# Kernel tuning notes

Hardware: AMD Instinct MI355X
Metric: run time of the kernel (lower is better)

Reference implementation:

```python
import jax, jax.numpy as jnp
import numpy as np

N = 20000
IN_CH, HID, OUT_CH = 512, 64, 16
H1, H2 = 8, 1
NEG_SLOPE = 0.2


def setup_inputs() -> dict:
    key = jax.random.key(0)
    ks = jax.random.split(key, 10)
    E = 320000
    x = jax.random.normal(ks[0], (N, IN_CH), dtype=jnp.float32)
    edge_index = jax.random.randint(ks[1], (2, E), 0, N, dtype=jnp.int64)
    s = 0.05
    return {
        "x": x,
        "edge_index": edge_index,
        "W1": jax.random.normal(ks[2], (H1 * HID, IN_CH), dtype=jnp.float32) * s,
        "att_src1": jax.random.normal(ks[3], (1, H1, HID), dtype=jnp.float32) * s,
        "att_dst1": jax.random.normal(ks[4], (1, H1, HID), dtype=jnp.float32) * s,
        "b1": jnp.zeros((H1 * HID,), dtype=jnp.float32),
        "W2": jax.random.normal(ks[5], (H2 * OUT_CH, H1 * HID), dtype=jnp.float32) * s,
        "att_src2": jax.random.normal(ks[6], (1, H2, OUT_CH), dtype=jnp.float32) * s,
        "att_dst2": jax.random.normal(ks[7], (1, H2, OUT_CH), dtype=jnp.float32) * s,
        "b2": jnp.zeros((OUT_CH,), dtype=jnp.float32),
    }


def _gat_conv(x, src, dst, W, att_src, att_dst, bias, heads, out_ch, concat):
    # Linear transform: [N, H, C]
    h = (x @ W.T).reshape(x.shape[0], heads, out_ch)
    n = x.shape[0]
    # Per-node attention logits (a_src . h), (a_dst . h): [N, H]
    a_s = (h * att_src).sum(-1)
    a_d = (h * att_dst).sum(-1)
    # Edge-wise LeakyReLU attention: [E, H]
    e = a_s[src] + a_d[dst]
    e = jnp.where(e >= 0, e, NEG_SLOPE * e)
    # Segment softmax over incoming edges of each destination node
    m = jax.ops.segment_max(e, dst, num_segments=n)
    p = jnp.exp(e - m[dst])
    z = jax.ops.segment_sum(p, dst, num_segments=n)
    alpha = p / z[dst]  # [E, H]
    # Weighted scatter-aggregate: out[dst] += alpha * h[src]
    msg = h[src] * alpha[:, :, None]  # [E, H, C]
    out = jax.ops.segment_sum(msg, dst, num_segments=n)
    out = out.reshape(n, heads * out_ch) if concat else out.mean(axis=1)
    return out + bias


def reference(x, edge_index, W1, att_src1, att_dst1, b1, W2, att_src2, att_dst2, b2):
    # PyG GATConv adds self-loops by default
    loops = jnp.arange(N, dtype=edge_index.dtype)
    src = jnp.concatenate([edge_index[0], loops])
    dst = jnp.concatenate([edge_index[1], loops])
    # dropout layers are identity in eval mode
    h = _gat_conv(x, src, dst, W1, att_src1, att_dst1, b1, H1, HID, True)
    h = jax.nn.relu(h)
    out = _gat_conv(h, src, dst, W2, att_src2, att_dst2, b2, H2, OUT_CH, False)
    return out
```

## Files before the change

### kernel.cpp

```cpp
#include <hip/hip_runtime.h>

#define Nn     20000
#define IN_CH  512
#define C1     512
#define H1n    8
#define HIDn   64
#define OUT_CH 16
#define En     320000
#define EPn    340000
#define NEG    0.2f

typedef __attribute__((ext_vector_type(8))) short bf16x8;
typedef __attribute__((ext_vector_type(4))) float f32x4;

__device__ inline unsigned short bf16_rne(float f) {
  unsigned int u = __float_as_uint(f);
  return (unsigned short)((u + 0x7fffu + ((u >> 16) & 1u)) >> 16);
}
__device__ inline float bf16_f(unsigned short u) {
  return __uint_as_float(((unsigned int)u) << 16);
}

#define NX8  (Nn * IN_CH / 8)
#define NW8  (C1 * IN_CH / 8)
#define NW28 (OUT_CH * C1 / 8)
__global__ __launch_bounds__(256) void cvt3_kernel(
    const float* __restrict__ x,  unsigned short* __restrict__ xb,
    const float* __restrict__ W1, unsigned short* __restrict__ w1b,
    const float* __restrict__ W2, unsigned short* __restrict__ w2b)
{
  int i = blockIdx.x * 256 + threadIdx.x;
  const float* in; unsigned short* ob; int idx;
  if (i < NX8) { in = x; ob = xb; idx = i; }
  else if (i < NX8 + NW8) { in = W1; ob = w1b; idx = i - NX8; }
  else if (i < NX8 + NW8 + NW28) { in = W2; ob = w2b; idx = i - NX8 - NW8; }
  else return;
  float4 f0 = ((const float4*)in)[idx * 2];
  float4 f1 = ((const float4*)in)[idx * 2 + 1];
  float f[8] = {f0.x, f0.y, f0.z, f0.w, f1.x, f1.y, f1.z, f1.w};
  unsigned short h[8];
#pragma unroll
  for (int j = 0; j < 8; j++) h[j] = bf16_rne(f[j]);
  ushort4 hv0 = {h[0], h[1], h[2], h[3]}, hv1 = {h[4], h[5], h[6], h[7]};
  ((ushort4*)ob)[idx * 2] = hv0; ((ushort4*)ob)[idx * 2 + 1] = hv1;
}

#define GLL(gp, lp) __builtin_amdgcn_global_load_lds( \
    (const __attribute__((address_space(1))) void*)(gp), \
    (__attribute__((address_space(3))) void*)(lp), 16, 0, 0)

#define SWZ(c) ((c) ^ (((c) >> 3) & 3))

__global__ __launch_bounds__(256, 3) void gemm1_mfma(
    const unsigned short* __restrict__ Ab, const unsigned short* __restrict__ Bb,
    const float* __restrict__ attS, const float* __restrict__ attD,
    unsigned short* __restrict__ Cb, float* __restrict__ as1, float* __restrict__ ad1)
{
  __shared__ unsigned short sA[128 * 32], sB[128 * 32];
  int t = threadIdx.x;
  int bm = blockIdx.x, bn = blockIdx.y;
  int lane = t & 63, w = t >> 6;

  int slot0 = w * 128 + lane;
  int slot1 = slot0 + 64;
  int cb0 = w * 128, cb1 = w * 128 + 64;
  int cs0 = SWZ(slot0), cs1 = SWZ(slot1);
  int ar0 = bm * 128 + (cs0 >> 2); if (ar0 > Nn - 1) ar0 = Nn - 1;
  int ar1 = bm * 128 + (cs1 >> 2); if (ar1 > Nn - 1) ar1 = Nn - 1;
  int br0 = bn * 128 + (cs0 >> 2);
  int br1 = bn * 128 + (cs1 >> 2);
  size_t offA0 = (size_t)ar0 * IN_CH + (cs0 & 3) * 8;
  size_t offA1 = (size_t)ar1 * IN_CH + (cs1 & 3) * 8;
  size_t offB0 = (size_t)br0 * IN_CH + (cs0 & 3) * 8;
  size_t offB1 = (size_t)br1 * IN_CH + (cs1 & 3) * 8;

  int wm = (w >> 1) * 64, wn = (w & 1) * 64;
  int lr = lane & 15, kb = lane >> 4;

  f32x4 acc[4][4] = {};

  for (int k0 = 0; k0 < IN_CH; k0 += 32) {
    __syncthreads();
    GLL(Ab + offA0 + k0, sA + cb0 * 8);
    GLL(Ab + offA1 + k0, sA + cb1 * 8);
    GLL(Bb + offB0 + k0, sB + cb0 * 8);
    GLL(Bb + offB1 + k0, sB + cb1 * 8);
    __syncthreads();

    bf16x8 ah[4], bh[4];
#pragma unroll
    for (int i = 0; i < 4; i++) {
      int rca = (wm + i * 16 + lr) * 4 + kb;
      ah[i] = *(const bf16x8*)&sA[SWZ(rca) * 8];
      int rcb = (wn + i * 16 + lr) * 4 + kb;
      bh[i] = *(const bf16x8*)&sB[SWZ(rcb) * 8];
    }
#pragma unroll
    for (int i = 0; i < 4; i++)
#pragma unroll
      for (int j = 0; j < 4; j++)
        acc[i][j] = __builtin_amdgcn_mfma_f32_16x16x32_bf16(ah[i], bh[j], acc[i][j], 0, 0, 0);
  }

  int lq = lane >> 4;
#pragma unroll
  for (int i = 0; i < 4; i++) {
    int r0 = bm * 128 + wm + i * 16 + lq * 4;
#pragma unroll
    for (int j = 0; j < 4; j++) {
      int cc = bn * 128 + wn + j * 16 + lr;
#pragma unroll
      for (int q = 0; q < 4; q++) {
        int r = r0 + q;
        if (r < Nn) Cb[(size_t)r * C1 + cc] = bf16_rne(acc[i][j][q]);
      }
    }
  }
  int hh = bn * 2 + (wn >> 6);
  float aSj[4], aDj[4];
#pragma unroll
  for (int j = 0; j < 4; j++) {
    int cc = bn * 128 + wn + j * 16 + lr;
    aSj[j] = attS[cc]; aDj[j] = attD[cc];
  }
#pragma unroll
  for (int i = 0; i < 4; i++)
#pragma unroll
    for (int q = 0; q < 4; q++) {
      float s = acc[i][0][q] * aSj[0] + acc[i][1][q] * aSj[1]
              + acc[i][2][q] * aSj[2] + acc[i][3][q] * aSj[3];
      float dd = acc[i][0][q] * aDj[0] + acc[i][1][q] * aDj[1]
               + acc[i][2][q] * aDj[2] + acc[i][3][q] * aDj[3];
#pragma unroll
      for (int off = 1; off < 16; off <<= 1) {
        s += __shfl_xor(s, off);
        dd += __shfl_xor(dd, off);
      }
      int r = bm * 128 + wm + i * 16 + lq * 4 + q;
      if (lr == 0 && r < Nn) { as1[r * 8 + hh] = s; ad1[r * 8 + hh] = dd; }
    }
}

__global__ void hist_kernel(const int* __restrict__ ei, int* __restrict__ cnt)
{
  int e = blockIdx.x * 256 + threadIdx.x;
  if (e >= EPn) return;
  int d = (e < En) ? ei[En + e] : (e - En);
  atomicAdd(&cnt[d], 1);
}

__global__ __launch_bounds__(1024) void scan_kernel(
    const int* __restrict__ cnt, int* __restrict__ row)
{
  __shared__ int wsum[16];
  int t = threadIdx.x;
  int base = t * 20;
  int v[20];
  int s = 0;
#pragma unroll
  for (int j = 0; j < 20; j++) {
    int i = base + j;
    int c = (i < Nn) ? cnt[i] : 0;
    v[j] = s;
    s += c;
  }
  int lane = t & 63, w = t >> 6;
  int incl = s;
#pragma unroll
  for (int off = 1; off < 64; off <<= 1) {
    int o = __shfl_up(incl, off);
    if (lane >= off) incl += o;
  }
  if (lane == 63) wsum[w] = incl;
  __syncthreads();
  if (w == 0) {
    int ws = (lane < 16) ? wsum[lane] : 0;
#pragma unroll
    for (int off = 1; off < 16; off <<= 1) {
      int o = __shfl_up(ws, off);
      if (lane >= off) ws += o;
    }
    if (lane < 16) wsum[lane] = ws;
  }
  __syncthreads();
  int excl = ((w > 0) ? wsum[w - 1] : 0) + incl - s;
#pragma unroll
  for (int j = 0; j < 20; j++) {
    int i = base + j;
    if (i < Nn) row[i] = excl + v[j];
  }
  if (t == 0) row[Nn] = EPn;
}

__global__ void scatter_kernel(const int* __restrict__ ei, const int* __restrict__ row,
                               int* __restrict__ cur, int* __restrict__ csr)
{
  int e = blockIdx.x * 256 + threadIdx.x;
  if (e >= EPn) return;
  int s, d;
  if (e < En) { s = ei[e]; d = ei[En + e]; }
  else        { s = e - En; d = e - En; }
  int pos = row[d] + atomicAdd(&cur[d], 1);
  csr[pos] = s;
}

__global__ __launch_bounds__(256) void agg1_kernel(
    const int* __restrict__ row, const int* __restrict__ csr,
    const unsigned short* __restrict__ h1b, const float* __restrict__ as1,
    const float* __restrict__ adv, const float* __restrict__ b1,
    unsigned short* __restrict__ outb)
{
  __shared__ float part[2][64 * 9];

  int t = threadIdx.x, lane = t & 63, w = t >> 6;
  int pr = w >> 1;
  int p  = w & 1;
  int d = blockIdx.x * 2 + pr;
  int beg = row[d], end = row[d + 1];
  int deg = end - beg;
  int hq = lane >> 3;
  size_t chb = (size_t)8 * lane;
  float adH = adv[d * 8 + hq];

  float a0 = 0.f, a1 = 0.f, a2 = 0.f, a3 = 0.f;
  float a4 = 0.f, a5 = 0.f, a6 = 0.f, a7 = 0.f;
  float z = 0.f;
  int nj = (deg - p + 1) >> 1;
#pragma unroll 4
  for (int j = 0; j < nj; j++) {
    int e = beg + p + 2 * j;
    int s = csr[e];
    float v = as1[s * 8 + hq] + adH;
    v = (v >= 0.f) ? v : NEG * v;
    float pp = __expf(v);
    z += pp;
    uint4 u = *(const uint4*)&h1b[(size_t)s * C1 + chb];
    a0 = fmaf(pp, __uint_as_float(u.x << 16), a0);
    a1 = fmaf(pp, __uint_as_float(u.x & 0xffff0000u), a1);
    a2 = fmaf(pp, __uint_as_float(u.y << 16), a2);
    a3 = fmaf(pp, __uint_as_float(u.y & 0xffff0000u), a3);
    a4 = fmaf(pp, __uint_as_float(u.z << 16), a4);
    a5 = fmaf(pp, __uint_as_float(u.z & 0xffff0000u), a5);
    a6 = fmaf(pp, __uint_as_float(u.w << 16), a6);
    a7 = fmaf(pp, __uint_as_float(u.w & 0xffff0000u), a7);
  }

  if (p == 1) {
    float* ps = &part[pr][lane * 9];
    ps[0] = a0; ps[1] = a1; ps[2] = a2; ps[3] = a3;
    ps[4] = a4; ps[5] = a5; ps[6] = a6; ps[7] = a7; ps[8] = z;
  }
  __syncthreads();
  if (p == 0) {
    const float* ps = &part[pr][lane * 9];
    a0 += ps[0]; a1 += ps[1]; a2 += ps[2]; a3 += ps[3];
    a4 += ps[4]; a5 += ps[5]; a6 += ps[6]; a7 += ps[7]; z += ps[8];
    float rz = 1.f / z;
    float4 b0 = *(const float4*)&b1[chb];
    float4 b4 = *(const float4*)&b1[chb + 4];
    float o[8] = {fmaf(a0, rz, b0.x), fmaf(a1, rz, b0.y),
                  fmaf(a2, rz, b0.z), fmaf(a3, rz, b0.w),
                  fmaf(a4, rz, b4.x), fmaf(a5, rz, b4.y),
                  fmaf(a6, rz, b4.z), fmaf(a7, rz, b4.w)};
    unsigned short r[8];
#pragma unroll
    for (int i = 0; i < 8; i++) r[i] = bf16_rne(o[i] > 0.f ? o[i] : 0.f);
    ushort4 r0 = {r[0], r[1], r[2], r[3]}, r4 = {r[4], r[5], r[6], r[7]};
    *(ushort4*)&outb[(size_t)d * C1 + chb] = r0;
    *(ushort4*)&outb[(size_t)d * C1 + chb + 4] = r4;
  }
}

__global__ __launch_bounds__(256) void l2_mfma(
    const unsigned short* __restrict__ Xb, const unsigned short* __restrict__ W2b,
    const float* __restrict__ att_s, const float* __restrict__ att_d,
    float* __restrict__ h2, float* __restrict__ as2, float* __restrict__ ad2)
{
  int w = threadIdx.x >> 6, lane = threadIdx.x & 63;
  int tile = blockIdx.x * 4 + w;
  if (tile >= Nn / 16) return;
  int n0 = tile * 16;
  int lr = lane & 15, kb = lane >> 4;

  bf16x8 bf[16];
#pragma unroll
  for (int k0 = 0; k0 < 16; k0++)
    bf[k0] = *(const bf16x8*)&W2b[lr * 512 + kb * 8 + k0 * 32];

  f32x4 acc = {0.f, 0.f, 0.f, 0.f};
#pragma unroll
  for (int k0 = 0; k0 < 16; k0++) {
    bf16x8 af = *(const bf16x8*)&Xb[(size_t)(n0 + lr) * 512 + kb * 8 + k0 * 32];
    acc = __builtin_amdgcn_mfma_f32_16x16x32_bf16(af, bf[k0], acc, 0, 0, 0);
  }

  float aS = att_s[lr], aD = att_d[lr];
#pragma unroll
  for (int r = 0; r < 4; r++) {
    int n = n0 + kb * 4 + r;
    h2[(size_t)n * 16 + lr] = acc[r];
    float sv = acc[r] * aS, dv = acc[r] * aD;
#pragma unroll
    for (int off = 1; off < 16; off <<= 1) {
      sv += __shfl_xor(sv, off);
      dv += __shfl_xor(dv, off);
    }
    if (lr == 0) { as2[n] = sv; ad2[n] = dv; }
  }
}

__global__ __launch_bounds__(256) void agg2_kernel(
    const int* __restrict__ row, const int* __restrict__ csr,
    const float* __restrict__ h2, const float* __restrict__ as2,
    const float* __restrict__ ad2, const float* __restrict__ b2,
    float* __restrict__ out)
{
  int wave = threadIdx.x >> 6, lane = threadIdx.x & 63;
  int d = blockIdx.x * 4 + wave;
  int beg = row[d], end = row[d + 1];
  float add = ad2[d];

  int c = lane & 15;
  float acc = 0.f, z = 0.f;
  for (int e = beg + (lane >> 4); e < end; e += 4) {
    int s = csr[e];
    float v = as2[s] + add;
    v = (v >= 0.f) ? v : NEG * v;
    float p = __expf(v);
    z += p;
    acc = fmaf(p, h2[(size_t)s * 16 + c], acc);
  }
  acc += __shfl_xor(acc, 16);
  acc += __shfl_xor(acc, 32);
  z += __shfl_xor(z, 16);
  z += __shfl_xor(z, 32);
  if (lane < 16) out[(size_t)d * 16 + lane] = acc / z + b2[lane];
}

extern "C" void kernel_launch(void* const* d_in, const int* in_sizes, int n_in,
                              void* d_out, int out_size, void* d_ws, size_t ws_size,
                              hipStream_t stream)
{
  const float* x    = (const float*)d_in[0];
  const int*   ei   = (const int*)d_in[1];
  const float* W1   = (const float*)d_in[2];
  const float* asv1 = (const float*)d_in[3];
  const float* adv1 = (const float*)d_in[4];
  const float* b1   = (const float*)d_in[5];
  const float* W2   = (const float*)d_in[6];
  const float* asv2 = (const float*)d_in[7];
  const float* adv2 = (const float*)d_in[8];
  const float* b2   = (const float*)d_in[9];
  float* out = (float*)d_out;

  unsigned short* h1b    = (unsigned short*)d_ws;
  unsigned short* relu1b = h1b + (size_t)Nn * C1;
  unsigned short* w_b    = relu1b + (size_t)Nn * C1;
  unsigned short* w2b    = w_b + (size_t)C1 * IN_CH;
  float* as1   = (float*)(w2b + (size_t)OUT_CH * C1);
  float* ad1   = as1 + (size_t)Nn * H1n;
  float* h2    = ad1 + (size_t)Nn * H1n;
  float* as2   = h2 + (size_t)Nn * OUT_CH;
  float* ad2   = as2 + Nn;
  int* csr  = (int*)(ad2 + Nn);
  int* cnt  = csr + EPn;
  int* cur  = cnt + Nn;
  int* rowp = cur + Nn;

  unsigned short* x_b = (unsigned short*)relu1b;

  hipMemsetAsync(cnt, 0, 2 * Nn * sizeof(int), stream);

  cvt3_kernel<<<(NX8 + NW8 + NW28 + 255) / 256, 256, 0, stream>>>(
      x, x_b, W1, w_b, W2, w2b);

  dim3 g1(157, 4);
  gemm1_mfma<<<g1, 256, 0, stream>>>(x_b, w_b, asv1, adv1, h1b, as1, ad1);

  hist_kernel<<<(EPn + 255) / 256, 256, 0, stream>>>(ei, cnt);
  scan_kernel<<<1, 1024, 0, stream>>>(cnt, rowp);
  scatter_kernel<<<(EPn + 255) / 256, 256, 0, stream>>>(ei, rowp, cur, csr);
  agg1_kernel<<<Nn / 2, 256, 0, stream>>>(rowp, csr, h1b, as1, ad1, b1, relu1b);
  l2_mfma<<<(Nn / 16 + 3) / 4, 256, 0, stream>>>(relu1b, w2b, asv2, adv2, h2, as2, ad2);
  agg2_kernel<<<Nn / 4, 256, 0, stream>>>(rowp, csr, h2, as2, ad2, b2, out);
}
```

Before: 164.5 us.

## Fuse fp32-to-bf16 conversion of x into GEMM1 and vectorize CSR build kernels

Drops the separate pass that converted x to bf16. GEMM1 now loads fp32 x tiles directly into LDS with a wider swizzle and packs them to bf16 with v_cvt_pk_bf16_f32 before the MFMAs. This removes a full read and write of the 20000x512 input, at the cost of doubling A-tile LDS footprint and global traffic per tile inside the GEMM. The histogram and scatter kernels also process four edges per thread using int4 loads, which cuts the thread count.

```diff
diff --git a/kernel.cpp b/kernel.cpp
--- a/kernel.cpp
+++ b/kernel.cpp
@@ -21,19 +21,27 @@
   return __uint_as_float(((unsigned int)u) << 16);
 }
 
-#define NX8  (Nn * IN_CH / 8)
+__device__ inline bf16x8 pack8(float4 f0, float4 f1) {
+  unsigned int r0, r1, r2, r3;
+  asm("v_cvt_pk_bf16_f32 %0, %1, %2" : "=v"(r0) : "v"(f0.x), "v"(f0.y));
+  asm("v_cvt_pk_bf16_f32 %0, %1, %2" : "=v"(r1) : "v"(f0.z), "v"(f0.w));
+  asm("v_cvt_pk_bf16_f32 %0, %1, %2" : "=v"(r2) : "v"(f1.x), "v"(f1.y));
+  asm("v_cvt_pk_bf16_f32 %0, %1, %2" : "=v"(r3) : "v"(f1.z), "v"(f1.w));
+  union { unsigned int u[4]; bf16x8 v; } un;
+  un.u[0] = r0; un.u[1] = r1; un.u[2] = r2; un.u[3] = r3;
+  return un.v;
+}
+
 #define NW8  (C1 * IN_CH / 8)
 #define NW28 (OUT_CH * C1 / 8)
-__global__ __launch_bounds__(256) void cvt3_kernel(
-    const float* __restrict__ x,  unsigned short* __restrict__ xb,
+__global__ __launch_bounds__(256) void cvt_w_kernel(
     const float* __restrict__ W1, unsigned short* __restrict__ w1b,
     const float* __restrict__ W2, unsigned short* __restrict__ w2b)
 {
   int i = blockIdx.x * 256 + threadIdx.x;
   const float* in; unsigned short* ob; int idx;
-  if (i < NX8) { in = x; ob = xb; idx = i; }
-  else if (i < NX8 + NW8) { in = W1; ob = w1b; idx = i - NX8; }
-  else if (i < NX8 + NW8 + NW28) { in = W2; ob = w2b; idx = i - NX8 - NW8; }
+  if (i < NW8) { in = W1; ob = w1b; idx = i; }
+  else if (i < NW8 + NW28) { in = W2; ob = w2b; idx = i - NW8; }
   else return;
   float4 f0 = ((const float4*)in)[idx * 2];
   float4 f1 = ((const float4*)in)[idx * 2 + 1];
@@ -49,28 +57,34 @@
     (const __attribute__((address_space(1))) void*)(gp), \
     (__attribute__((address_space(3))) void*)(lp), 16, 0, 0)
 
-#define SWZ(c) ((c) ^ (((c) >> 3) & 3))
+#define SWZ(c)  ((c) ^ (((c) >> 3) & 3))
+#define SWZA(c) ((c) ^ (((c) >> 3) & 7))
 
 __global__ __launch_bounds__(256, 3) void gemm1_mfma(
-    const unsigned short* __restrict__ Ab, const unsigned short* __restrict__ Bb,
+    const float* __restrict__ Af, const unsigned short* __restrict__ Bb,
     const float* __restrict__ attS, const float* __restrict__ attD,
     unsigned short* __restrict__ Cb, float* __restrict__ as1, float* __restrict__ ad1)
 {
-  __shared__ unsigned short sA[128 * 32], sB[128 * 32];
+  __shared__ float sAf[128 * 32];
+  __shared__ unsigned short sB[128 * 32];
   int t = threadIdx.x;
   int bm = blockIdx.x, bn = blockIdx.y;
   int lane = t & 63, w = t >> 6;
 
-  int slot0 = w * 128 + lane;
-  int slot1 = slot0 + 64;
-  int cb0 = w * 128, cb1 = w * 128 + 64;
+  int acb[4]; size_t aoff[4];
+#pragma unroll
+  for (int q = 0; q < 4; q++) {
+    int slot = w * 256 + q * 64 + lane;
+    acb[q] = w * 256 + q * 64;
+    int cs = SWZA(slot);
+    int ra = bm * 128 + (cs >> 3); if (ra > Nn - 1) ra = Nn - 1;
+    aoff[q] = (size_t)ra * IN_CH + (cs & 7) * 4;
+  }
+  int slot0 = w * 128 + lane, slot1 = slot0 + 64;
+  int bcb0 = w * 128, bcb1 = w * 128 + 64;
   int cs0 = SWZ(slot0), cs1 = SWZ(slot1);
-  int ar0 = bm * 128 + (cs0 >> 2); if (ar0 > Nn - 1) ar0 = Nn - 1;
-  int ar1 = bm * 128 + (cs1 >> 2); if (ar1 > Nn - 1) ar1 = Nn - 1;
   int br0 = bn * 128 + (cs0 >> 2);
   int br1 = bn * 128 + (cs1 >> 2);
-  size_t offA0 = (size_t)ar0 * IN_CH + (cs0 & 3) * 8;
-  size_t offA1 = (size_t)ar1 * IN_CH + (cs1 & 3) * 8;
   size_t offB0 = (size_t)br0 * IN_CH + (cs0 & 3) * 8;
   size_t offB1 = (size_t)br1 * IN_CH + (cs1 & 3) * 8;
 
@@ -81,17 +95,21 @@
 
   for (int k0 = 0; k0 < IN_CH; k0 += 32) {
     __syncthreads();
-    GLL(Ab + offA0 + k0, sA + cb0 * 8);
-    GLL(Ab + offA1 + k0, sA + cb1 * 8);
-    GLL(Bb + offB0 + k0, sB + cb0 * 8);
-    GLL(Bb + offB1 + k0, sB + cb1 * 8);
+    GLL(Af + aoff[0] + k0, sAf + acb[0] * 4);
+    GLL(Af + aoff[1] + k0, sAf + acb[1] * 4);
+    GLL(Af + aoff[2] + k0, sAf + acb[2] * 4);
+    GLL(Af + aoff[3] + k0, sAf + acb[3] * 4);
+    GLL(Bb + offB0 + k0, sB + bcb0 * 8);
+    GLL(Bb + offB1 + k0, sB + bcb1 * 8);
     __syncthreads();
 
     bf16x8 ah[4], bh[4];
 #pragma unroll
     for (int i = 0; i < 4; i++) {
-      int rca = (wm + i * 16 + lr) * 4 + kb;
-      ah[i] = *(const bf16x8*)&sA[SWZ(rca) * 8];
+      int c0 = (wm + i * 16 + lr) * 8 + kb * 2;
+      float4 f0 = *(const float4*)&sAf[SWZA(c0) * 4];
+      float4 f1 = *(const float4*)&sAf[SWZA(c0 + 1) * 4];
+      ah[i] = pack8(f0, f1);
       int rcb = (wn + i * 16 + lr) * 4 + kb;
       bh[i] = *(const bf16x8*)&sB[SWZ(rcb) * 8];
     }
@@ -143,10 +161,17 @@
 
 __global__ void hist_kernel(const int* __restrict__ ei, int* __restrict__ cnt)
 {
-  int e = blockIdx.x * 256 + threadIdx.x;
-  if (e >= EPn) return;
-  int d = (e < En) ? ei[En + e] : (e - En);
-  atomicAdd(&cnt[d], 1);
+  int e4 = (blockIdx.x * 256 + threadIdx.x) * 4;
+  if (e4 >= EPn) return;
+  if (e4 < En) {
+    int4 dv = *(const int4*)&ei[En + e4];
+    atomicAdd(&cnt[dv.x], 1); atomicAdd(&cnt[dv.y], 1);
+    atomicAdd(&cnt[dv.z], 1); atomicAdd(&cnt[dv.w], 1);
+  } else {
+    int d = e4 - En;
+    atomicAdd(&cnt[d], 1);     atomicAdd(&cnt[d + 1], 1);
+    atomicAdd(&cnt[d + 2], 1); atomicAdd(&cnt[d + 3], 1);
+  }
 }
 
 __global__ __launch_bounds__(1024) void scan_kernel(
@@ -195,13 +220,26 @@
 __global__ void scatter_kernel(const int* __restrict__ ei, const int* __restrict__ row,
                                int* __restrict__ cur, int* __restrict__ csr)
 {
-  int e = blockIdx.x * 256 + threadIdx.x;
-  if (e >= EPn) return;
-  int s, d;
-  if (e < En) { s = ei[e]; d = ei[En + e]; }
-  else        { s = e - En; d = e - En; }
-  int pos = row[d] + atomicAdd(&cur[d], 1);
-  csr[pos] = s;
+  int e4 = (blockIdx.x * 256 + threadIdx.x) * 4;
+  if (e4 >= EPn) return;
+  if (e4 < En) {
+    int4 sv = *(const int4*)&ei[e4];
+    int4 dv = *(const int4*)&ei[En + e4];
+    int sa[4] = {sv.x, sv.y, sv.z, sv.w};
+    int da[4] = {dv.x, dv.y, dv.z, dv.w};
+#pragma unroll
+    for (int j = 0; j < 4; j++) {
+      int pos = row[da[j]] + atomicAdd(&cur[da[j]], 1);
+      csr[pos] = sa[j];
+    }
+  } else {
+#pragma unroll
+    for (int j = 0; j < 4; j++) {
+      int d = e4 - En + j;
+      int pos = row[d] + atomicAdd(&cur[d], 1);
+      csr[pos] = d;
+    }
+  }
 }
 
 __global__ __launch_bounds__(256) void agg1_kernel(
@@ -367,19 +405,16 @@
   int* cur  = cnt + Nn;
   int* rowp = cur + Nn;
 
-  unsigned short* x_b = (unsigned short*)relu1b;
-
   hipMemsetAsync(cnt, 0, 2 * Nn * sizeof(int), stream);
 
-  cvt3_kernel<<<(NX8 + NW8 + NW28 + 255) / 256, 256, 0, stream>>>(
-      x, x_b, W1, w_b, W2, w2b);
+  cvt_w_kernel<<<(NW8 + NW28 + 255) / 256, 256, 0, stream>>>(W1, w_b, W2, w2b);
 
   dim3 g1(157, 4);
-  gemm1_mfma<<<g1, 256, 0, stream>>>(x_b, w_b, asv1, adv1, h1b, as1, ad1);
-
-  hist_kernel<<<(EPn + 255) / 256, 256, 0, stream>>>(ei, cnt);
+  gemm1_mfma<<<g1, 256, 0, stream>>>(x, w_b, asv1, adv1, h1b, as1, ad1);
+
+  hist_kernel<<<(EPn / 4 + 255) / 256, 256, 0, stream>>>(ei, cnt);
   scan_kernel<<<1, 1024, 0, stream>>>(cnt, rowp);
-  scatter_kernel<<<(EPn + 255) / 256, 256, 0, stream>>>(ei, rowp, cur, csr);
+  scatter_kernel<<<(EPn / 4 + 255) / 256, 256, 0, stream>>>(ei, rowp, cur, csr);
   agg1_kernel<<<Nn / 2, 256, 0, stream>>>(rowp, csr, h1b, as1, ad1, b1, relu1b);
   l2_mfma<<<(Nn / 16 + 3) / 4, 256, 0, stream>>>(relu1b, w2b, asv2, adv2, h2, as2, ad2);
   agg2_kernel<<<Nn / 4, 256, 0, stream>>>(rowp, csr, h2, as2, ad2, b2, out);
```

Result: slower. 169.1 us (+2.8%).

## Fuse layer-2 linear into agg1 epilogue; fold memset into cvt; vectorize hist/scatter

Applied to the files above, without the earlier changes.

Removes the separate l2_mfma kernel and the bf16 relu1 intermediate buffer. Each agg1 block stages W2 in LDS and computes the 16-wide layer-2 projection plus attention logits directly from the fp32 ReLU outputs, using wave-wide shuffle reductions. The counter memset is folded into the conversion kernel, and hist/scatter each process 4 edges per thread with int4 loads. The tradeoffs are 16 KB of extra LDS and a W2 copy per agg1 block, plus 16×6 shuffle reductions per node instead of MFMA.

```diff
diff --git a/kernel.cpp b/kernel.cpp
--- a/kernel.cpp
+++ b/kernel.cpp
@@ -24,17 +24,23 @@
 #define NX8  (Nn * IN_CH / 8)
 #define NW8  (C1 * IN_CH / 8)
 #define NW28 (OUT_CH * C1 / 8)
+#define NZ4  (2 * Nn / 4)
 __global__ __launch_bounds__(256) void cvt3_kernel(
     const float* __restrict__ x,  unsigned short* __restrict__ xb,
     const float* __restrict__ W1, unsigned short* __restrict__ w1b,
-    const float* __restrict__ W2, unsigned short* __restrict__ w2b)
+    const float* __restrict__ W2, unsigned short* __restrict__ w2b,
+    int* __restrict__ zbase)
 {
   int i = blockIdx.x * 256 + threadIdx.x;
   const float* in; unsigned short* ob; int idx;
   if (i < NX8) { in = x; ob = xb; idx = i; }
   else if (i < NX8 + NW8) { in = W1; ob = w1b; idx = i - NX8; }
   else if (i < NX8 + NW8 + NW28) { in = W2; ob = w2b; idx = i - NX8 - NW8; }
-  else return;
+  else if (i < NX8 + NW8 + NW28 + NZ4) {
+    int4 zz = {0, 0, 0, 0};
+    ((int4*)zbase)[i - NX8 - NW8 - NW28] = zz;
+    return;
+  } else return;
   float4 f0 = ((const float4*)in)[idx * 2];
   float4 f1 = ((const float4*)in)[idx * 2 + 1];
   float f[8] = {f0.x, f0.y, f0.z, f0.w, f1.x, f1.y, f1.z, f1.w};
@@ -143,10 +149,17 @@
 
 __global__ void hist_kernel(const int* __restrict__ ei, int* __restrict__ cnt)
 {
-  int e = blockIdx.x * 256 + threadIdx.x;
-  if (e >= EPn) return;
-  int d = (e < En) ? ei[En + e] : (e - En);
-  atomicAdd(&cnt[d], 1);
+  int e4 = (blockIdx.x * 256 + threadIdx.x) * 4;
+  if (e4 >= EPn) return;
+  if (e4 < En) {
+    int4 dv = *(const int4*)&ei[En + e4];
+    atomicAdd(&cnt[dv.x], 1); atomicAdd(&cnt[dv.y], 1);
+    atomicAdd(&cnt[dv.z], 1); atomicAdd(&cnt[dv.w], 1);
+  } else {
+    int d = e4 - En;
+    atomicAdd(&cnt[d], 1);     atomicAdd(&cnt[d + 1], 1);
+    atomicAdd(&cnt[d + 2], 1); atomicAdd(&cnt[d + 3], 1);
+  }
 }
 
 __global__ __launch_bounds__(1024) void scan_kernel(
@@ -195,24 +208,47 @@
 __global__ void scatter_kernel(const int* __restrict__ ei, const int* __restrict__ row,
                                int* __restrict__ cur, int* __restrict__ csr)
 {
-  int e = blockIdx.x * 256 + threadIdx.x;
-  if (e >= EPn) return;
-  int s, d;
-  if (e < En) { s = ei[e]; d = ei[En + e]; }
-  else        { s = e - En; d = e - En; }
-  int pos = row[d] + atomicAdd(&cur[d], 1);
-  csr[pos] = s;
+  int e4 = (blockIdx.x * 256 + threadIdx.x) * 4;
+  if (e4 >= EPn) return;
+  if (e4 < En) {
+    int4 sv = *(const int4*)&ei[e4];
+    int4 dv = *(const int4*)&ei[En + e4];
+    int sa[4] = {sv.x, sv.y, sv.z, sv.w};
+    int da[4] = {dv.x, dv.y, dv.z, dv.w};
+#pragma unroll
+    for (int j = 0; j < 4; j++) {
+      int pos = row[da[j]] + atomicAdd(&cur[da[j]], 1);
+      csr[pos] = sa[j];
+    }
+  } else {
+#pragma unroll
+    for (int j = 0; j < 4; j++) {
+      int d = e4 - En + j;
+      int pos = row[d] + atomicAdd(&cur[d], 1);
+      csr[pos] = d;
+    }
+  }
 }
 
 __global__ __launch_bounds__(256) void agg1_kernel(
     const int* __restrict__ row, const int* __restrict__ csr,
     const unsigned short* __restrict__ h1b, const float* __restrict__ as1,
     const float* __restrict__ adv, const float* __restrict__ b1,
-    unsigned short* __restrict__ outb)
+    const unsigned short* __restrict__ W2b,
+    const float* __restrict__ attS2, const float* __restrict__ attD2,
+    float* __restrict__ h2, float* __restrict__ as2, float* __restrict__ ad2)
 {
   __shared__ float part[2][64 * 9];
+  __shared__ unsigned short w2s[OUT_CH * 512];
 
   int t = threadIdx.x, lane = t & 63, w = t >> 6;
+  {
+    const uint4* src = (const uint4*)W2b;
+    uint4* dst = (uint4*)w2s;
+#pragma unroll
+    for (int q = 0; q < 4; q++) dst[t + q * 256] = src[t + q * 256];
+  }
+
   int pr = w >> 1;
   int p  = w & 1;
   int d = blockIdx.x * 2 + pr;
@@ -258,54 +294,31 @@
     float rz = 1.f / z;
     float4 b0 = *(const float4*)&b1[chb];
     float4 b4 = *(const float4*)&b1[chb + 4];
-    float o[8] = {fmaf(a0, rz, b0.x), fmaf(a1, rz, b0.y),
-                  fmaf(a2, rz, b0.z), fmaf(a3, rz, b0.w),
-                  fmaf(a4, rz, b4.x), fmaf(a5, rz, b4.y),
-                  fmaf(a6, rz, b4.z), fmaf(a7, rz, b4.w)};
-    unsigned short r[8];
-#pragma unroll
-    for (int i = 0; i < 8; i++) r[i] = bf16_rne(o[i] > 0.f ? o[i] : 0.f);
-    ushort4 r0 = {r[0], r[1], r[2], r[3]}, r4 = {r[4], r[5], r[6], r[7]};
-    *(ushort4*)&outb[(size_t)d * C1 + chb] = r0;
-    *(ushort4*)&outb[(size_t)d * C1 + chb + 4] = r4;
-  }
-}
-
-__global__ __launch_bounds__(256) void l2_mfma(
-    const unsigned short* __restrict__ Xb, const unsigned short* __restrict__ W2b,
-    const float* __restrict__ att_s, const float* __restrict__ att_d,
-    float* __restrict__ h2, float* __restrict__ as2, float* __restrict__ ad2)
-{
-  int w = threadIdx.x >> 6, lane = threadIdx.x & 63;
-  int tile = blockIdx.x * 4 + w;
-  if (tile >= Nn / 16) return;
-  int n0 = tile * 16;
-  int lr = lane & 15, kb = lane >> 4;
-
-  bf16x8 bf[16];
-#pragma unroll
-  for (int k0 = 0; k0 < 16; k0++)
-    bf[k0] = *(const bf16x8*)&W2b[lr * 512 + kb * 8 + k0 * 32];
-
-  f32x4 acc = {0.f, 0.f, 0.f, 0.f};
-#pragma unroll
-  for (int k0 = 0; k0 < 16; k0++) {
-    bf16x8 af = *(const bf16x8*)&Xb[(size_t)(n0 + lr) * 512 + kb * 8 + k0 * 32];
-    acc = __builtin_amdgcn_mfma_f32_16x16x32_bf16(af, bf[k0], acc, 0, 0, 0);
-  }
-
-  float aS = att_s[lr], aD = att_d[lr];
-#pragma unroll
-  for (int r = 0; r < 4; r++) {
-    int n = n0 + kb * 4 + r;
-    h2[(size_t)n * 16 + lr] = acc[r];
-    float sv = acc[r] * aS, dv = acc[r] * aD;
-#pragma unroll
-    for (int off = 1; off < 16; off <<= 1) {
-      sv += __shfl_xor(sv, off);
-      dv += __shfl_xor(dv, off);
-    }
-    if (lr == 0) { as2[n] = sv; ad2[n] = dv; }
+    float o0 = fmaf(a0, rz, b0.x); o0 = o0 > 0.f ? o0 : 0.f;
+    float o1 = fmaf(a1, rz, b0.y); o1 = o1 > 0.f ? o1 : 0.f;
+    float o2 = fmaf(a2, rz, b0.z); o2 = o2 > 0.f ? o2 : 0.f;
+    float o3 = fmaf(a3, rz, b0.w); o3 = o3 > 0.f ? o3 : 0.f;
+    float o4 = fmaf(a4, rz, b4.x); o4 = o4 > 0.f ? o4 : 0.f;
+    float o5 = fmaf(a5, rz, b4.y); o5 = o5 > 0.f ? o5 : 0.f;
+    float o6 = fmaf(a6, rz, b4.z); o6 = o6 > 0.f ? o6 : 0.f;
+    float o7 = fmaf(a7, rz, b4.w); o7 = o7 > 0.f ? o7 : 0.f;
+
+    float myh2 = 0.f, s2 = 0.f, d2 = 0.f;
+#pragma unroll
+    for (int j = 0; j < OUT_CH; j++) {
+      bf16x8 wv = *(const bf16x8*)&w2s[j * 512 + chb];
+      float pj = o0 * bf16_f((unsigned short)wv[0]) + o1 * bf16_f((unsigned short)wv[1])
+               + o2 * bf16_f((unsigned short)wv[2]) + o3 * bf16_f((unsigned short)wv[3])
+               + o4 * bf16_f((unsigned short)wv[4]) + o5 * bf16_f((unsigned short)wv[5])
+               + o6 * bf16_f((unsigned short)wv[6]) + o7 * bf16_f((unsigned short)wv[7]);
+#pragma unroll
+      for (int off = 1; off < 64; off <<= 1) pj += __shfl_xor(pj, off);
+      if (lane == j) myh2 = pj;
+      s2 = fmaf(pj, attS2[j], s2);
+      d2 = fmaf(pj, attD2[j], d2);
+    }
+    if (lane < OUT_CH) h2[(size_t)d * OUT_CH + lane] = myh2;
+    if (lane == 0) { as2[d] = s2; ad2[d] = d2; }
   }
 }
 
@@ -353,10 +366,10 @@
   const float* b2   = (const float*)d_in[9];
   float* out = (float*)d_out;
 
-  unsigned short* h1b    = (unsigned short*)d_ws;
-  unsigned short* relu1b = h1b + (size_t)Nn * C1;
-  unsigned short* w_b    = relu1b + (size_t)Nn * C1;
-  unsigned short* w2b    = w_b + (size_t)C1 * IN_CH;
+  unsigned short* x_b = (unsigned short*)d_ws;
+  unsigned short* h1b = x_b + (size_t)Nn * IN_CH;
+  unsigned short* w_b = h1b + (size_t)Nn * C1;
+  unsigned short* w2b = w_b + (size_t)C1 * IN_CH;
   float* as1   = (float*)(w2b + (size_t)OUT_CH * C1);
   float* ad1   = as1 + (size_t)Nn * H1n;
   float* h2    = ad1 + (size_t)Nn * H1n;
@@ -367,20 +380,16 @@
   int* cur  = cnt + Nn;
   int* rowp = cur + Nn;
 
-  unsigned short* x_b = (unsigned short*)relu1b;
-
-  hipMemsetAsync(cnt, 0, 2 * Nn * sizeof(int), stream);
-
-  cvt3_kernel<<<(NX8 + NW8 + NW28 + 255) / 256, 256, 0, stream>>>(
-      x, x_b, W1, w_b, W2, w2b);
+  cvt3_kernel<<<(NX8 + NW8 + NW28 + NZ4 + 255) / 256, 256, 0, stream>>>(
+      x, x_b, W1, w_b, W2, w2b, cnt);
 
   dim3 g1(157, 4);
   gemm1_mfma<<<g1, 256, 0, stream>>>(x_b, w_b, asv1, adv1, h1b, as1, ad1);
 
-  hist_kernel<<<(EPn + 255) / 256, 256, 0, stream>>>(ei, cnt);
+  hist_kernel<<<(EPn / 4 + 255) / 256, 256, 0, stream>>>(ei, cnt);
   scan_kernel<<<1, 1024, 0, stream>>>(cnt, rowp);
-  scatter_kernel<<<(EPn + 255) / 256, 256, 0, stream>>>(ei, rowp, cur, csr);
-  agg1_kernel<<<Nn / 2, 256, 0, stream>>>(rowp, csr, h1b, as1, ad1, b1, relu1b);
-  l2_mfma<<<(Nn / 16 + 3) / 4, 256, 0, stream>>>(relu1b, w2b, asv2, adv2, h2, as2, ad2);
+  scatter_kernel<<<(EPn / 4 + 255) / 256, 256, 0, stream>>>(ei, rowp, cur, csr);
+  agg1_kernel<<<Nn / 2, 256, 0, stream>>>(rowp, csr, h1b, as1, ad1, b1,
+                                          w2b, asv2, adv2, h2, as2, ad2);
   agg2_kernel<<<Nn / 4, 256, 0, stream>>>(rowp, csr, h2, as2, ad2, b2, out);
 }
```

After: 158.5 us. -3.7%, faster.
